# Kernel tuning notes

Measured on AMD Instinct MI355X. Metric: run time of the kernel, lower is better.

Reference implementation:

```python
import jax, jax.numpy as jnp
import numpy as np

GROUPS = 8
NUM_HEADS = 8
EPS = 1e-5


def setup_inputs() -> dict:
    key = jax.random.key(0)
    ks = jax.random.split(key, 3)
    C = 512
    x = jax.random.normal(ks[0], (2, C, 64, 64), dtype=jnp.float32)
    norm_w = jnp.ones((C,), jnp.float32)
    norm_b = jnp.zeros((C,), jnp.float32)
    qkv_w = jax.random.normal(ks[1], (3 * C, C), dtype=jnp.float32) * (C ** -0.5)
    qkv_b = jnp.zeros((3 * C,), jnp.float32)
    proj_w = jax.random.normal(ks[2], (C, C), dtype=jnp.float32) * (C ** -0.5)
    proj_b = jnp.zeros((C,), jnp.float32)
    return {"x": x, "norm_w": norm_w, "norm_b": norm_b,
            "qkv_w": qkv_w, "qkv_b": qkv_b,
            "proj_w": proj_w, "proj_b": proj_b}


def reference(x, norm_w, norm_b, qkv_w, qkv_b, proj_w, proj_b):
    b, c, h, w = x.shape
    n = h * w
    hd = c // NUM_HEADS

    # GroupNorm(8, c): normalize over (channels-in-group, h, w)
    xg = x.reshape(b, GROUPS, c // GROUPS, h, w)
    mean = jnp.mean(xg, axis=(2, 3, 4), keepdims=True)
    var = jnp.var(xg, axis=(2, 3, 4), keepdims=True)
    xg = (xg - mean) * jax.lax.rsqrt(var + EPS)
    x_norm = xg.reshape(b, c, h, w) * norm_w[None, :, None, None] + norm_b[None, :, None, None]

    x_flat = x_norm.reshape(b, c, n)  # (b, c, n)
    # 1x1 Conv1d == channel-wise linear
    qkv = jnp.einsum('oc,bcn->bon', qkv_w, x_flat) + qkv_b[None, :, None]
    q, k, v = jnp.split(qkv, 3, axis=1)
    q = q.reshape(b, NUM_HEADS, hd, n)
    k = k.reshape(b, NUM_HEADS, hd, n)
    v = v.reshape(b, NUM_HEADS, hd, n)

    attn = jnp.einsum('bhdn,bhdm->bhnm', q, k) * (hd ** -0.5)  # (b,h,n,n)
    attn = jax.nn.softmax(attn, axis=-1)
    out = jnp.einsum('bhnm,bhdm->bhdn', attn, v).reshape(b, c, n)

    out = jnp.einsum('oc,bcn->bon', proj_w, out) + proj_b[None, :, None]
    return x + out.reshape(b, c, h, w)
```

## Files before the change

### kernel.cpp

```cpp
#include <hip/hip_runtime.h>
#include <stdint.h>

#define B_   2
#define C_   512
#define N_   4096
#define G_   8
#define NH_  8
#define HD_  64
#define GRPELEMS ((C_ / G_) * N_)
#define NCHUNK 16

typedef __bf16 bf16x8 __attribute__((ext_vector_type(8)));
typedef float  f32x4  __attribute__((ext_vector_type(4)));

#if __has_builtin(__builtin_amdgcn_exp2f)
#define EXP2(x) __builtin_amdgcn_exp2f(x)
#else
#define EXP2(x) exp2f(x)
#endif

__device__ inline unsigned f2bf(float f) {
    union { float f; unsigned u; } v; v.f = f;
    return (v.u + 0x7FFFu + ((v.u >> 16) & 1u)) >> 16;
}
__device__ inline __bf16 tobf(float f) {
    unsigned short u = (unsigned short)f2bf(f);
    union { unsigned short u; __bf16 b; } c; c.u = u;
    return c.b;
}
__device__ inline unsigned pktrunc(float f0, float f1) {
    return __builtin_amdgcn_perm(__float_as_uint(f1), __float_as_uint(f0),
                                 0x07060302u);
}
__device__ inline float trunc_bf(float f) {
    return __uint_as_float(__float_as_uint(f) & 0xffff0000u);
}

#define GLOAD16(g, l)                                                     \
    __builtin_amdgcn_global_load_lds(                                     \
        (const __attribute__((address_space(1))) unsigned*)(g),           \
        (__attribute__((address_space(3))) unsigned*)(l), 16, 0, 0)

__global__ __launch_bounds__(256) void prep(const float* __restrict__ x,
                                            const float* __restrict__ qw,
                                            const float* __restrict__ pw,
                                            float* __restrict__ psum,
                                            float* __restrict__ psq,
                                            __bf16* __restrict__ dq,
                                            __bf16* __restrict__ dp) {
    const int blk = blockIdx.x;
    const int t = threadIdx.x;
    if (blk < 256) {
        const float4* p = (const float4*)x + (size_t)blk * 4096;
        float s = 0.f, s2 = 0.f;
#pragma unroll
        for (int i = 0; i < 16; ++i) {
            float4 v = p[t + (i << 8)];
            s  += v.x + v.y + v.z + v.w;
            s2 += v.x * v.x + v.y * v.y + v.z * v.z + v.w * v.w;
        }
#pragma unroll
        for (int off = 1; off < 64; off <<= 1) {
            s  += __shfl_xor(s, off);
            s2 += __shfl_xor(s2, off);
        }
        __shared__ float rs[4], rq[4];
        if ((t & 63) == 0) { rs[t >> 6] = s; rq[t >> 6] = s2; }
        __syncthreads();
        if (t == 0) {
            psum[blk] = rs[0] + rs[1] + rs[2] + rs[3];
            psq[blk]  = rq[0] + rq[1] + rq[2] + rq[3];
        }
    } else {
        const int QW4 = (3 * C_ * C_) / 4;
        int idx = (blk - 256) * 256 + t;
        float4 v; __bf16* dst; int o;
        if (idx < QW4) { v = ((const float4*)qw)[idx]; dst = dq; o = idx; }
        else           { v = ((const float4*)pw)[idx - QW4]; dst = dp; o = idx - QW4; }
        uint2 pk;
        pk.x = f2bf(v.x) | (f2bf(v.y) << 16);
        pk.y = f2bf(v.z) | (f2bf(v.w) << 16);
        *(uint2*)(dst + (size_t)o * 4) = pk;
    }
}

__global__ __launch_bounds__(256) void gn_apply_t(const float* __restrict__ x,
                                                  const float* __restrict__ w,
                                                  const float* __restrict__ bb,
                                                  const float* __restrict__ psum,
                                                  const float* __restrict__ psq,
                                                  __bf16* __restrict__ xnT) {
    const int p0 = blockIdx.x << 6, c0 = blockIdx.y << 6, b = blockIdx.z;
    __shared__ __bf16 T[64][76];
    __shared__ float red[2 * NCHUNK];
    __shared__ float smr[2];
    const int tid = threadIdx.x;
    const int bg = b * G_ + (c0 >> 6);

    if (tid < NCHUNK)            red[tid] = psum[bg * NCHUNK + tid];
    else if (tid < 2 * NCHUNK)   red[tid] = psq[bg * NCHUNK + tid - NCHUNK];
    __syncthreads();
    if (tid == 0) {
        float s = 0.f, q = 0.f;
#pragma unroll
        for (int i = 0; i < NCHUNK; ++i) { s += red[i]; q += red[NCHUNK + i]; }
        const float inv = 1.f / (float)GRPELEMS;
        float mean = s * inv;
        float var  = q * inv - mean * mean;
        smr[0] = mean;
        smr[1] = rsqrtf(var + 1e-5f);
    }
    __syncthreads();
    const float mean = smr[0], rstd = smr[1];

    const int tr  = tid >> 4;
    const int tc4 = (tid & 15) << 2;
    const float* xb = x + ((size_t)b * C_ + c0) * N_ + p0;
#pragma unroll
    for (int cc = tr; cc < 64; cc += 16) {
        int c = c0 + cc;
        float sc = rstd * w[c];
        float sh = bb[c] - mean * sc;
        float4 v = *(const float4*)(xb + (size_t)cc * N_ + tc4);
        T[tc4 + 0][cc] = tobf(v.x * sc + sh);
        T[tc4 + 1][cc] = tobf(v.y * sc + sh);
        T[tc4 + 2][cc] = tobf(v.z * sc + sh);
        T[tc4 + 3][cc] = tobf(v.w * sc + sh);
    }
    __syncthreads();
    __bf16* dst = xnT + ((size_t)b * N_ + p0) * C_ + c0;
#pragma unroll
    for (int pp = tr; pp < 64; pp += 16)
        *(uint2*)(dst + (size_t)pp * C_ + tc4) = *(const uint2*)&T[pp][tc4];
}

template <int M_TOTAL, int EPI>
__global__ __launch_bounds__(256) void gemm_bf16(const __bf16* __restrict__ A,
                                                 const __bf16* __restrict__ Bm,
                                                 const float* __restrict__ bias,
                                                 const float* __restrict__ resid,
                                                 __bf16* __restrict__ qT,
                                                 __bf16* __restrict__ kP,
                                                 __bf16* __restrict__ vP,
                                                 float* __restrict__ Y) {
    const int b  = blockIdx.z;
    const int M0 = blockIdx.y << 7;
    const int N0 = blockIdx.x << 7;
    const int tid = threadIdx.x;
    const int w = tid >> 6, lane = tid & 63;
    const int quad = lane >> 4, l16 = lane & 15;
    const int wr = w >> 1, wc = w & 1;

    __shared__ __bf16 As[128 * 64];
    __shared__ __bf16 Bs[128 * 64];

    const __bf16* Bb = Bm + (size_t)b * ((size_t)N_ * C_);

    const int srow = lane >> 3;
    const int sg   = lane & 7;

    f32x4 acc[4][4];
#pragma unroll
    for (int mt = 0; mt < 4; ++mt)
#pragma unroll
        for (int nt = 0; nt < 4; ++nt) acc[mt][nt] = (f32x4){0.f, 0.f, 0.f, 0.f};

    for (int k0 = 0; k0 < C_; k0 += 64) {
        __syncthreads();
#pragma unroll
        for (int i = 0; i < 4; ++i) {
            int r  = (w << 5) + (i << 3) + srow;
            int gc = ((sg ^ (r & 7)) << 3);
            const __bf16* ga = A  + (size_t)(M0 + r) * C_ + k0 + gc;
            const __bf16* gb = Bb + (size_t)(N0 + r) * C_ + k0 + gc;
            GLOAD16(ga, As + (((w << 2) + i) << 9));
            GLOAD16(gb, Bs + (((w << 2) + i) << 9));
        }
        __syncthreads();

#pragma unroll
        for (int kk = 0; kk < 2; ++kk) {
            bf16x8 af[4], bfr[4];
            const int gk = (kk << 2) + quad;
#pragma unroll
            for (int mt = 0; mt < 4; ++mt) {
                int m = (wr << 6) + (mt << 4) + l16;
                af[mt] = *(const bf16x8*)&As[(m << 6) + ((gk ^ (m & 7)) << 3)];
            }
#pragma unroll
            for (int nt = 0; nt < 4; ++nt) {
                int n = (wc << 6) + (nt << 4) + l16;
                bfr[nt] = *(const bf16x8*)&Bs[(n << 6) + ((gk ^ (n & 7)) << 3)];
            }
#pragma unroll
            for (int mt = 0; mt < 4; ++mt)
#pragma unroll
                for (int nt = 0; nt < 4; ++nt)
                    acc[mt][nt] = __builtin_amdgcn_mfma_f32_16x16x32_bf16(
                        af[mt], bfr[nt], acc[mt][nt], 0, 0, 0);
        }
    }

    if (EPI == 0) {
        const int t = M0 >> 9;
        const float sc = (t == 0) ? (0.125f * 1.44269504f) : 1.f;
#pragma unroll
        for (int mt = 0; mt < 4; ++mt) {
            const int o0 = M0 + (wr << 6) + (mt << 4) + (quad << 2);
            const int h  = (o0 >> 6) & 7;
            const int d0 = o0 & 63;
            const size_t bh = (size_t)b * NH_ + h;
            float bi[4];
#pragma unroll
            for (int r = 0; r < 4; ++r) bi[r] = bias[o0 + r];
            if (t == 0) {
                __bf16* dst = qT + (bh * N_) * HD_ + d0;
#pragma unroll
                for (int nt = 0; nt < 4; ++nt) {
                    int p = N0 + (wc << 6) + (nt << 4) + l16;
                    f32x4 v = acc[mt][nt];
                    uint2 pk;
                    pk.x = f2bf((v[0] + bi[0]) * sc) | (f2bf((v[1] + bi[1]) * sc) << 16);
                    pk.y = f2bf((v[2] + bi[2]) * sc) | (f2bf((v[3] + bi[3]) * sc) << 16);
                    *(uint2*)(dst + (size_t)p * HD_) = pk;
                }
            } else if (t == 1) {
                __bf16* dst = kP + bh * ((size_t)N_ * HD_);
                const size_t kkbase = (size_t)(d0 >> 3) * N_;
                const int rem = d0 & 7;
#pragma unroll
                for (int nt = 0; nt < 4; ++nt) {
                    int p = N0 + (wc << 6) + (nt << 4) + l16;
                    f32x4 v = acc[mt][nt];
                    uint2 pk;
                    pk.x = f2bf(v[0] + bi[0]) | (f2bf(v[1] + bi[1]) << 16);
                    pk.y = f2bf(v[2] + bi[2]) | (f2bf(v[3] + bi[3]) << 16);
                    *(uint2*)(dst + (kkbase + p) * 8 + rem) = pk;
                }
            } else {
                __bf16* dst = vP + bh * ((size_t)HD_ * N_);
#pragma unroll
                for (int nt = 0; nt < 4; ++nt) {
                    int p = N0 + (wc << 6) + (nt << 4) + l16;
                    const size_t gb2 = ((size_t)(p >> 3) * HD_) * 8 + (p & 7);
                    f32x4 v = acc[mt][nt];
#pragma unroll
                    for (int r = 0; r < 4; ++r)
                        dst[gb2 + (size_t)(d0 + r) * 8] = tobf(v[r] + bi[r]);
                }
            }
        }
    } else {
#pragma unroll
        for (int mt = 0; mt < 4; ++mt) {
            const int o0 = M0 + (wr << 6) + (mt << 4) + (quad << 2);
            float bi[4];
#pragma unroll
            for (int r = 0; r < 4; ++r) bi[r] = bias[o0 + r];
#pragma unroll
            for (int nt = 0; nt < 4; ++nt) {
                int p = N0 + (wc << 6) + (nt << 4) + l16;
                f32x4 v = acc[mt][nt];
#pragma unroll
                for (int r = 0; r < 4; ++r) {
                    size_t off = ((size_t)b * C_ + o0 + r) * N_ + p;
                    Y[off] = v[r] + bi[r] + resid[off];
                }
            }
        }
    }
}

__global__ __launch_bounds__(256) void attn_mfma(const __bf16* __restrict__ qT,
                                                 const __bf16* __restrict__ kP,
                                                 const __bf16* __restrict__ vP,
                                                 __bf16* __restrict__ attT) {
    const int tid  = threadIdx.x;
    const int w    = tid >> 6;
    const int lane = tid & 63;
    const int quad = lane >> 4;
    const int l16  = lane & 15;
    const int l7   = l16 & 7;
    const int h = blockIdx.y, b = blockIdx.z;
    const int qw0 = (blockIdx.x << 7) + (w << 5);

    __shared__ __bf16 Ps[4][32][64];

    const size_t bh = (size_t)b * NH_ + h;
    const __bf16* qTb = qT + bh * ((size_t)N_ * HD_);
    const __bf16* kPb = kP + bh * ((size_t)N_ * HD_);
    const __bf16* vPb = vP + bh * ((size_t)HD_ * N_);

    bf16x8 qf[2][2];
#pragma unroll
    for (int qt = 0; qt < 2; ++qt)
#pragma unroll
        for (int hh = 0; hh < 2; ++hh)
            qf[qt][hh] = *(const bf16x8*)(qTb +
                (size_t)(qw0 + (qt << 4) + l16) * HD_ + (hh << 5) + (quad << 3));

#define KADDR(hh, kt, kb) (kPb + (((size_t)((hh << 2) + quad) * N_) + (kb) + ((kt) << 4) + l16) * 8)
#define VADDR(h2, dt, kb) (vPb + (((size_t)(((kb) >> 3) + ((h2) << 2) + quad) * HD_) + ((dt) << 4) + l16) * 8)

    const f32x4 zero4 = {0.f, 0.f, 0.f, 0.f};
    f32x4 o[4][2];
#pragma unroll
    for (int dt = 0; dt < 4; ++dt) { o[dt][0] = zero4; o[dt][1] = zero4; }
    float lacc[2] = {0.f, 0.f};

    bf16x8 kf[2][4];
#pragma unroll
    for (int hh = 0; hh < 2; ++hh)
#pragma unroll
        for (int kt = 0; kt < 4; ++kt)
            kf[hh][kt] = *(const bf16x8*)KADDR(hh, kt, 0);

    for (int it = 0; it < 64; ++it) {
        const int kb = it << 6;

        bf16x8 vf[2][4];
#pragma unroll
        for (int h2 = 0; h2 < 2; ++h2)
#pragma unroll
            for (int dt = 0; dt < 4; ++dt)
                vf[h2][dt] = *(const bf16x8*)VADDR(h2, dt, kb);

        f32x4 s[4][2];
#pragma unroll
        for (int kt = 0; kt < 4; ++kt) { s[kt][0] = zero4; s[kt][1] = zero4; }
#pragma unroll
        for (int hh = 0; hh < 2; ++hh)
#pragma unroll
            for (int kt = 0; kt < 4; ++kt) {
                s[kt][0] = __builtin_amdgcn_mfma_f32_16x16x32_bf16(
                    kf[hh][kt], qf[0][hh], s[kt][0], 0, 0, 0);
                s[kt][1] = __builtin_amdgcn_mfma_f32_16x16x32_bf16(
                    kf[hh][kt], qf[1][hh], s[kt][1], 0, 0, 0);
            }

#pragma unroll
        for (int qt = 0; qt < 2; ++qt)
#pragma unroll
            for (int kt = 0; kt < 4; ++kt) {
                f32x4 sv = s[kt][qt];
                float e0 = EXP2(sv[0]), e1 = EXP2(sv[1]);
                float e2 = EXP2(sv[2]), e3 = EXP2(sv[3]);
                lacc[qt] += (trunc_bf(e0) + trunc_bf(e1)) +
                            (trunc_bf(e2) + trunc_bf(e3));
                uint2 pk;
                pk.x = pktrunc(e0, e1);
                pk.y = pktrunc(e2, e3);
                *(uint2*)&Ps[w][(qt << 4) + l16]
                            [(((kt << 2) + quad) ^ (l7 << 1)) << 2] = pk;
            }

        if (it < 63) {
#pragma unroll
            for (int hh = 0; hh < 2; ++hh)
#pragma unroll
                for (int kt = 0; kt < 4; ++kt)
                    kf[hh][kt] = *(const bf16x8*)KADDR(hh, kt, kb + 64);
        }

#pragma unroll
        for (int hh = 0; hh < 2; ++hh) {
            bf16x8 pf0 = *(const bf16x8*)&Ps[w][l16]
                          [(((hh << 3) + (quad << 1)) ^ (l7 << 1)) << 2];
            bf16x8 pf1 = *(const bf16x8*)&Ps[w][16 + l16]
                          [(((hh << 3) + (quad << 1)) ^ (l7 << 1)) << 2];
#pragma unroll
            for (int dt = 0; dt < 4; ++dt) {
                o[dt][0] = __builtin_amdgcn_mfma_f32_16x16x32_bf16(
                    vf[hh][dt], pf0, o[dt][0], 0, 0, 0);
                o[dt][1] = __builtin_amdgcn_mfma_f32_16x16x32_bf16(
                    vf[hh][dt], pf1, o[dt][1], 0, 0, 0);
            }
        }
    }

    float lq[2];
#pragma unroll
    for (int qt = 0; qt < 2; ++qt) {
        float v = lacc[qt];
        v += __shfl_xor(v, 16);
        v += __shfl_xor(v, 32);
        lq[qt] = v;
    }

#pragma unroll
    for (int qt = 0; qt < 2; ++qt) {
        float inv = 1.f / lq[qt];
        int n = qw0 + (qt << 4) + l16;
        __bf16* dst = attT + ((size_t)b * N_ + n) * C_ + h * HD_ + (quad << 2);
#pragma unroll
        for (int dt = 0; dt < 4; ++dt) {
            uint2 pk;
            pk.x = f2bf(o[dt][qt][0] * inv) | (f2bf(o[dt][qt][1] * inv) << 16);
            pk.y = f2bf(o[dt][qt][2] * inv) | (f2bf(o[dt][qt][3] * inv) << 16);
            *(uint2*)(dst + (dt << 4)) = pk;
        }
    }
#undef KADDR
#undef VADDR
}

extern "C" void kernel_launch(void* const* d_in, const int* in_sizes, int n_in,
                              void* d_out, int out_size, void* d_ws, size_t ws_size,
                              hipStream_t stream) {
    const float* x      = (const float*)d_in[0];
    const float* norm_w = (const float*)d_in[1];
    const float* norm_b = (const float*)d_in[2];
    const float* qkv_w  = (const float*)d_in[3];
    const float* qkv_b  = (const float*)d_in[4];
    const float* proj_w = (const float*)d_in[5];
    const float* proj_b = (const float*)d_in[6];
    float* out = (float*)d_out;

    const size_t BCN = (size_t)B_ * C_ * N_;
    float* psum  = (float*)d_ws;
    float* psq   = psum + 256;
    __bf16* xnT  = (__bf16*)(psq + 256);
    __bf16* qT   = xnT + BCN;
    __bf16* kP   = qT + BCN;
    __bf16* vP   = kP + BCN;
    __bf16* attT = vP + BCN;
    __bf16* wq   = attT + BCN;
    __bf16* wp   = wq + (size_t)3 * C_ * C_;

    prep<<<1280, 256, 0, stream>>>(x, qkv_w, proj_w, psum, psq, wq, wp);
    gn_apply_t<<<dim3(N_ / 64, C_ / 64, B_), 256, 0, stream>>>(
        x, norm_w, norm_b, psum, psq, xnT);
    gemm_bf16<3 * C_, 0><<<dim3(N_ / 128, 3 * C_ / 128, B_), 256, 0, stream>>>(
        wq, xnT, qkv_b, nullptr, qT, kP, vP, nullptr);
    attn_mfma<<<dim3(N_ / 128, NH_, B_), 256, 0, stream>>>(qT, kP, vP, attT);
    gemm_bf16<C_, 1><<<dim3(N_ / 128, C_ / 128, B_), 256, 0, stream>>>(
        wp, attT, proj_b, x, nullptr, nullptr, nullptr, out);
}
```

Measured before the change: 215.9 us.

## Tile K/V into contiguous 64-key blocks and halve attention query tile per wave

The QKV GEMM epilogue now writes K and V in 64-key blocks of 4096 contiguous bf16 elements, so each attention iteration reads one contiguous chunk and advances the pointer. The attention kernel drops from 32 to 16 queries per wave, doubling the grid to 1024 blocks. The softmax row sum is now an extra MFMA against a ones vector instead of scalar adds plus shuffles. The smaller query tile means each K/V load feeds half as many MFMAs, so global traffic per unit of compute roughly doubles in exchange for more blocks and fewer registers per wave.

```diff
diff --git a/kernel.cpp b/kernel.cpp
--- a/kernel.cpp
+++ b/kernel.cpp
@@ -31,9 +31,6 @@
 __device__ inline unsigned pktrunc(float f0, float f1) {
     return __builtin_amdgcn_perm(__float_as_uint(f1), __float_as_uint(f0),
                                  0x07060302u);
-}
-__device__ inline float trunc_bf(float f) {
-    return __uint_as_float(__float_as_uint(f) & 0xffff0000u);
 }
 
 #define GLOAD16(g, l)                                                     \
@@ -226,8 +223,6 @@
                 }
             } else if (t == 1) {
                 __bf16* dst = kP + bh * ((size_t)N_ * HD_);
-                const size_t kkbase = (size_t)(d0 >> 3) * N_;
-                const int rem = d0 & 7;
 #pragma unroll
                 for (int nt = 0; nt < 4; ++nt) {
                     int p = N0 + (wc << 6) + (nt << 4) + l16;
@@ -235,18 +230,21 @@
                     uint2 pk;
                     pk.x = f2bf(v[0] + bi[0]) | (f2bf(v[1] + bi[1]) << 16);
                     pk.y = f2bf(v[2] + bi[2]) | (f2bf(v[3] + bi[3]) << 16);
-                    *(uint2*)(dst + (kkbase + p) * 8 + rem) = pk;
+                    size_t off = (size_t)(p >> 6) * 4096 +
+                                 (size_t)((d0 >> 3) * 64 + (p & 63)) * 8 + (d0 & 7);
+                    *(uint2*)(dst + off) = pk;
                 }
             } else {
                 __bf16* dst = vP + bh * ((size_t)HD_ * N_);
 #pragma unroll
                 for (int nt = 0; nt < 4; ++nt) {
                     int p = N0 + (wc << 6) + (nt << 4) + l16;
-                    const size_t gb2 = ((size_t)(p >> 3) * HD_) * 8 + (p & 7);
+                    size_t base = (size_t)(p >> 6) * 4096 +
+                                  (size_t)(((p >> 3) & 7) * 64) * 8 + (p & 7);
                     f32x4 v = acc[mt][nt];
 #pragma unroll
                     for (int r = 0; r < 4; ++r)
-                        dst[gb2 + (size_t)(d0 + r) * 8] = tobf(v[r] + bi[r]);
+                        dst[base + (size_t)(d0 + r) * 8] = tobf(v[r] + bi[r]);
                 }
             }
         }
@@ -282,126 +280,107 @@
     const int l16  = lane & 15;
     const int l7   = l16 & 7;
     const int h = blockIdx.y, b = blockIdx.z;
-    const int qw0 = (blockIdx.x << 7) + (w << 5);
-
-    __shared__ __bf16 Ps[4][32][64];
+    const int qw0 = (blockIdx.x << 6) + (w << 4);
+
+    __shared__ __bf16 Ps[4][16][64];
 
     const size_t bh = (size_t)b * NH_ + h;
     const __bf16* qTb = qT + bh * ((size_t)N_ * HD_);
-    const __bf16* kPb = kP + bh * ((size_t)N_ * HD_);
-    const __bf16* vPb = vP + bh * ((size_t)HD_ * N_);
-
-    bf16x8 qf[2][2];
-#pragma unroll
-    for (int qt = 0; qt < 2; ++qt)
+    const __bf16* kblk = kP + bh * ((size_t)N_ * HD_);
+    const __bf16* vblk = vP + bh * ((size_t)HD_ * N_);
+
+    const int voff0 = (quad * 64 + l16) * 8;
+    const int voff1 = ((4 + quad) * 64 + l16) * 8;
+
+    bf16x8 qf[2];
+#pragma unroll
+    for (int hh = 0; hh < 2; ++hh)
+        qf[hh] = *(const bf16x8*)(qTb +
+            (size_t)(qw0 + l16) * HD_ + (hh << 5) + (quad << 3));
+
+    bf16x8 ones;
+#pragma unroll
+    for (int i = 0; i < 8; ++i) ones[i] = (__bf16)1.0f;
+
+    const f32x4 zero4 = {0.f, 0.f, 0.f, 0.f};
+    f32x4 o[4];
+#pragma unroll
+    for (int dt = 0; dt < 4; ++dt) o[dt] = zero4;
+    f32x4 o4 = zero4;
+
+    bf16x8 kf[2][4];
+#pragma unroll
+    for (int hh = 0; hh < 2; ++hh)
+#pragma unroll
+        for (int kt = 0; kt < 4; ++kt)
+            kf[hh][kt] = *(const bf16x8*)(kblk + (hh ? voff1 : voff0) + (kt << 7));
+
+    for (int it = 0; it < 64; ++it) {
+        bf16x8 vf[2][4];
+#pragma unroll
+        for (int h2 = 0; h2 < 2; ++h2)
+#pragma unroll
+            for (int dt = 0; dt < 4; ++dt)
+                vf[h2][dt] = *(const bf16x8*)(vblk + (h2 ? voff1 : voff0) + (dt << 7));
+
+        f32x4 s[4];
+#pragma unroll
+        for (int kt = 0; kt < 4; ++kt) s[kt] = zero4;
 #pragma unroll
         for (int hh = 0; hh < 2; ++hh)
-            qf[qt][hh] = *(const bf16x8*)(qTb +
-                (size_t)(qw0 + (qt << 4) + l16) * HD_ + (hh << 5) + (quad << 3));
-
-#define KADDR(hh, kt, kb) (kPb + (((size_t)((hh << 2) + quad) * N_) + (kb) + ((kt) << 4) + l16) * 8)
-#define VADDR(h2, dt, kb) (vPb + (((size_t)(((kb) >> 3) + ((h2) << 2) + quad) * HD_) + ((dt) << 4) + l16) * 8)
-
-    const f32x4 zero4 = {0.f, 0.f, 0.f, 0.f};
-    f32x4 o[4][2];
-#pragma unroll
-    for (int dt = 0; dt < 4; ++dt) { o[dt][0] = zero4; o[dt][1] = zero4; }
-    float lacc[2] = {0.f, 0.f};
-
-    bf16x8 kf[2][4];
-#pragma unroll
-    for (int hh = 0; hh < 2; ++hh)
-#pragma unroll
-        for (int kt = 0; kt < 4; ++kt)
-            kf[hh][kt] = *(const bf16x8*)KADDR(hh, kt, 0);
-
-    for (int it = 0; it < 64; ++it) {
-        const int kb = it << 6;
-
-        bf16x8 vf[2][4];
-#pragma unroll
-        for (int h2 = 0; h2 < 2; ++h2)
+#pragma unroll
+            for (int kt = 0; kt < 4; ++kt)
+                s[kt] = __builtin_amdgcn_mfma_f32_16x16x32_bf16(
+                    kf[hh][kt], qf[hh], s[kt], 0, 0, 0);
+
+#pragma unroll
+        for (int kt = 0; kt < 4; ++kt) {
+            f32x4 sv = s[kt];
+            float e0 = EXP2(sv[0]), e1 = EXP2(sv[1]);
+            float e2 = EXP2(sv[2]), e3 = EXP2(sv[3]);
+            uint2 pk;
+            pk.x = pktrunc(e0, e1);
+            pk.y = pktrunc(e2, e3);
+            *(uint2*)&Ps[w][l16][(((kt << 2) + quad) ^ (l7 << 1)) << 2] = pk;
+        }
+
+        if (it < 63) {
+            const __bf16* knext = kblk + 4096;
+#pragma unroll
+            for (int hh = 0; hh < 2; ++hh)
+#pragma unroll
+                for (int kt = 0; kt < 4; ++kt)
+                    kf[hh][kt] = *(const bf16x8*)(knext + (hh ? voff1 : voff0) + (kt << 7));
+        }
+
+#pragma unroll
+        for (int hh = 0; hh < 2; ++hh) {
+            bf16x8 pf = *(const bf16x8*)&Ps[w][l16]
+                          [(((hh << 3) + (quad << 1)) ^ (l7 << 1)) << 2];
 #pragma unroll
             for (int dt = 0; dt < 4; ++dt)
-                vf[h2][dt] = *(const bf16x8*)VADDR(h2, dt, kb);
-
-        f32x4 s[4][2];
-#pragma unroll
-        for (int kt = 0; kt < 4; ++kt) { s[kt][0] = zero4; s[kt][1] = zero4; }
-#pragma unroll
-        for (int hh = 0; hh < 2; ++hh)
-#pragma unroll
-            for (int kt = 0; kt < 4; ++kt) {
-                s[kt][0] = __builtin_amdgcn_mfma_f32_16x16x32_bf16(
-                    kf[hh][kt], qf[0][hh], s[kt][0], 0, 0, 0);
-                s[kt][1] = __builtin_amdgcn_mfma_f32_16x16x32_bf16(
-                    kf[hh][kt], qf[1][hh], s[kt][1], 0, 0, 0);
-            }
-
-#pragma unroll
-        for (int qt = 0; qt < 2; ++qt)
-#pragma unroll
-            for (int kt = 0; kt < 4; ++kt) {
-                f32x4 sv = s[kt][qt];
-                float e0 = EXP2(sv[0]), e1 = EXP2(sv[1]);
-                float e2 = EXP2(sv[2]), e3 = EXP2(sv[3]);
-                lacc[qt] += (trunc_bf(e0) + trunc_bf(e1)) +
-                            (trunc_bf(e2) + trunc_bf(e3));
-                uint2 pk;
-                pk.x = pktrunc(e0, e1);
-                pk.y = pktrunc(e2, e3);
-                *(uint2*)&Ps[w][(qt << 4) + l16]
-                            [(((kt << 2) + quad) ^ (l7 << 1)) << 2] = pk;
-            }
-
-        if (it < 63) {
-#pragma unroll
-            for (int hh = 0; hh < 2; ++hh)
-#pragma unroll
-                for (int kt = 0; kt < 4; ++kt)
-                    kf[hh][kt] = *(const bf16x8*)KADDR(hh, kt, kb + 64);
-        }
-
-#pragma unroll
-        for (int hh = 0; hh < 2; ++hh) {
-            bf16x8 pf0 = *(const bf16x8*)&Ps[w][l16]
-                          [(((hh << 3) + (quad << 1)) ^ (l7 << 1)) << 2];
-            bf16x8 pf1 = *(const bf16x8*)&Ps[w][16 + l16]
-                          [(((hh << 3) + (quad << 1)) ^ (l7 << 1)) << 2];
-#pragma unroll
-            for (int dt = 0; dt < 4; ++dt) {
-                o[dt][0] = __builtin_amdgcn_mfma_f32_16x16x32_bf16(
-                    vf[hh][dt], pf0, o[dt][0], 0, 0, 0);
-                o[dt][1] = __builtin_amdgcn_mfma_f32_16x16x32_bf16(
-                    vf[hh][dt], pf1, o[dt][1], 0, 0, 0);
-            }
-        }
-    }
-
-    float lq[2];
-#pragma unroll
-    for (int qt = 0; qt < 2; ++qt) {
-        float v = lacc[qt];
-        v += __shfl_xor(v, 16);
-        v += __shfl_xor(v, 32);
-        lq[qt] = v;
-    }
-
-#pragma unroll
-    for (int qt = 0; qt < 2; ++qt) {
-        float inv = 1.f / lq[qt];
-        int n = qw0 + (qt << 4) + l16;
+                o[dt] = __builtin_amdgcn_mfma_f32_16x16x32_bf16(
+                    vf[hh][dt], pf, o[dt], 0, 0, 0);
+            o4 = __builtin_amdgcn_mfma_f32_16x16x32_bf16(ones, pf, o4, 0, 0, 0);
+        }
+
+        kblk += 4096;
+        vblk += 4096;
+    }
+
+    const float inv = 1.f / o4[0];
+
+    {
+        int n = qw0 + l16;
         __bf16* dst = attT + ((size_t)b * N_ + n) * C_ + h * HD_ + (quad << 2);
 #pragma unroll
         for (int dt = 0; dt < 4; ++dt) {
             uint2 pk;
-            pk.x = f2bf(o[dt][qt][0] * inv) | (f2bf(o[dt][qt][1] * inv) << 16);
-            pk.y = f2bf(o[dt][qt][2] * inv) | (f2bf(o[dt][qt][3] * inv) << 16);
+            pk.x = f2bf(o[dt][0] * inv) | (f2bf(o[dt][1] * inv) << 16);
+            pk.y = f2bf(o[dt][2] * inv) | (f2bf(o[dt][3] * inv) << 16);
             *(uint2*)(dst + (dt << 4)) = pk;
         }
     }
-#undef KADDR
-#undef VADDR
 }
 
 extern "C" void kernel_launch(void* const* d_in, const int* in_sizes, int n_in,
@@ -432,7 +411,7 @@
         x, norm_w, norm_b, psum, psq, xnT);
     gemm_bf16<3 * C_, 0><<<dim3(N_ / 128, 3 * C_ / 128, B_), 256, 0, stream>>>(
         wq, xnT, qkv_b, nullptr, qT, kP, vP, nullptr);
-    attn_mfma<<<dim3(N_ / 128, NH_, B_), 256, 0, stream>>>(qT, kP, vP, attT);
+    attn_mfma<<<dim3(N_ / 64, NH_, B_), 256, 0, stream>>>(qT, kP, vP, attT);
     gemm_bf16<C_, 1><<<dim3(N_ / 128, C_ / 128, B_), 256, 0, stream>>>(
         wp, attT, proj_b, x, nullptr, nullptr, nullptr, out);
 }
```

New measurement: 263.6 us. +22.1%, slower.

## Tile K/V into contiguous 64-key blocks and compute softmax row sums via MFMA

Applied to the files above, without the earlier changes.

Changes the K and V packed layouts so each 64-key block is a contiguous 4096-element chunk, which turns the attention loop's address math into pointer increments and keeps each iteration's loads within one contiguous region. It also removes the per-element truncate-and-add softmax denominator accumulation and the cross-lane shuffles, replacing them with an extra MFMA against a ones vector on the P tiles already held in registers. This trades VALU work for two more MFMAs per half-iteration and requires the QKV epilogue to write the new layout.

```diff
diff --git a/kernel.cpp b/kernel.cpp
--- a/kernel.cpp
+++ b/kernel.cpp
@@ -31,9 +31,6 @@
 __device__ inline unsigned pktrunc(float f0, float f1) {
     return __builtin_amdgcn_perm(__float_as_uint(f1), __float_as_uint(f0),
                                  0x07060302u);
-}
-__device__ inline float trunc_bf(float f) {
-    return __uint_as_float(__float_as_uint(f) & 0xffff0000u);
 }
 
 #define GLOAD16(g, l)                                                     \
@@ -226,8 +223,6 @@
                 }
             } else if (t == 1) {
                 __bf16* dst = kP + bh * ((size_t)N_ * HD_);
-                const size_t kkbase = (size_t)(d0 >> 3) * N_;
-                const int rem = d0 & 7;
 #pragma unroll
                 for (int nt = 0; nt < 4; ++nt) {
                     int p = N0 + (wc << 6) + (nt << 4) + l16;
@@ -235,18 +230,21 @@
                     uint2 pk;
                     pk.x = f2bf(v[0] + bi[0]) | (f2bf(v[1] + bi[1]) << 16);
                     pk.y = f2bf(v[2] + bi[2]) | (f2bf(v[3] + bi[3]) << 16);
-                    *(uint2*)(dst + (kkbase + p) * 8 + rem) = pk;
+                    size_t off = (size_t)(p >> 6) * 4096 +
+                                 (size_t)((d0 >> 3) * 64 + (p & 63)) * 8 + (d0 & 7);
+                    *(uint2*)(dst + off) = pk;
                 }
             } else {
                 __bf16* dst = vP + bh * ((size_t)HD_ * N_);
 #pragma unroll
                 for (int nt = 0; nt < 4; ++nt) {
                     int p = N0 + (wc << 6) + (nt << 4) + l16;
-                    const size_t gb2 = ((size_t)(p >> 3) * HD_) * 8 + (p & 7);
+                    size_t base = (size_t)(p >> 6) * 4096 +
+                                  (size_t)(((p >> 3) & 7) * 64) * 8 + (p & 7);
                     f32x4 v = acc[mt][nt];
 #pragma unroll
                     for (int r = 0; r < 4; ++r)
-                        dst[gb2 + (size_t)(d0 + r) * 8] = tobf(v[r] + bi[r]);
+                        dst[base + (size_t)(d0 + r) * 8] = tobf(v[r] + bi[r]);
                 }
             }
         }
@@ -287,9 +285,12 @@
     __shared__ __bf16 Ps[4][32][64];
 
     const size_t bh = (size_t)b * NH_ + h;
-    const __bf16* qTb = qT + bh * ((size_t)N_ * HD_);
-    const __bf16* kPb = kP + bh * ((size_t)N_ * HD_);
-    const __bf16* vPb = vP + bh * ((size_t)HD_ * N_);
+    const __bf16* qTb  = qT + bh * ((size_t)N_ * HD_);
+    const __bf16* kblk = kP + bh * ((size_t)N_ * HD_);
+    const __bf16* vblk = vP + bh * ((size_t)HD_ * N_);
+
+    const int voff0 = (quad * 64 + l16) * 8;
+    const int voff1 = ((4 + quad) * 64 + l16) * 8;
 
     bf16x8 qf[2][2];
 #pragma unroll
@@ -299,31 +300,30 @@
             qf[qt][hh] = *(const bf16x8*)(qTb +
                 (size_t)(qw0 + (qt << 4) + l16) * HD_ + (hh << 5) + (quad << 3));
 
-#define KADDR(hh, kt, kb) (kPb + (((size_t)((hh << 2) + quad) * N_) + (kb) + ((kt) << 4) + l16) * 8)
-#define VADDR(h2, dt, kb) (vPb + (((size_t)(((kb) >> 3) + ((h2) << 2) + quad) * HD_) + ((dt) << 4) + l16) * 8)
+    bf16x8 ones;
+#pragma unroll
+    for (int i = 0; i < 8; ++i) ones[i] = (__bf16)1.0f;
 
     const f32x4 zero4 = {0.f, 0.f, 0.f, 0.f};
     f32x4 o[4][2];
 #pragma unroll
     for (int dt = 0; dt < 4; ++dt) { o[dt][0] = zero4; o[dt][1] = zero4; }
-    float lacc[2] = {0.f, 0.f};
+    f32x4 ol[2] = {zero4, zero4};
 
     bf16x8 kf[2][4];
 #pragma unroll
     for (int hh = 0; hh < 2; ++hh)
 #pragma unroll
         for (int kt = 0; kt < 4; ++kt)
-            kf[hh][kt] = *(const bf16x8*)KADDR(hh, kt, 0);
+            kf[hh][kt] = *(const bf16x8*)(kblk + (hh ? voff1 : voff0) + (kt << 7));
 
     for (int it = 0; it < 64; ++it) {
-        const int kb = it << 6;
-
         bf16x8 vf[2][4];
 #pragma unroll
         for (int h2 = 0; h2 < 2; ++h2)
 #pragma unroll
             for (int dt = 0; dt < 4; ++dt)
-                vf[h2][dt] = *(const bf16x8*)VADDR(h2, dt, kb);
+                vf[h2][dt] = *(const bf16x8*)(vblk + (h2 ? voff1 : voff0) + (dt << 7));
 
         f32x4 s[4][2];
 #pragma unroll
@@ -345,8 +345,6 @@
                 f32x4 sv = s[kt][qt];
                 float e0 = EXP2(sv[0]), e1 = EXP2(sv[1]);
                 float e2 = EXP2(sv[2]), e3 = EXP2(sv[3]);
-                lacc[qt] += (trunc_bf(e0) + trunc_bf(e1)) +
-                            (trunc_bf(e2) + trunc_bf(e3));
                 uint2 pk;
                 pk.x = pktrunc(e0, e1);
                 pk.y = pktrunc(e2, e3);
@@ -355,11 +353,12 @@
             }
 
         if (it < 63) {
+            const __bf16* knext = kblk + 4096;
 #pragma unroll
             for (int hh = 0; hh < 2; ++hh)
 #pragma unroll
                 for (int kt = 0; kt < 4; ++kt)
-                    kf[hh][kt] = *(const bf16x8*)KADDR(hh, kt, kb + 64);
+                    kf[hh][kt] = *(const bf16x8*)(knext + (hh ? voff1 : voff0) + (kt << 7));
         }
 
 #pragma unroll
@@ -375,21 +374,17 @@
                 o[dt][1] = __builtin_amdgcn_mfma_f32_16x16x32_bf16(
                     vf[hh][dt], pf1, o[dt][1], 0, 0, 0);
             }
-        }
-    }
-
-    float lq[2];
+            ol[0] = __builtin_amdgcn_mfma_f32_16x16x32_bf16(ones, pf0, ol[0], 0, 0, 0);
+            ol[1] = __builtin_amdgcn_mfma_f32_16x16x32_bf16(ones, pf1, ol[1], 0, 0, 0);
+        }
+
+        kblk += 4096;
+        vblk += 4096;
+    }
+
 #pragma unroll
     for (int qt = 0; qt < 2; ++qt) {
-        float v = lacc[qt];
-        v += __shfl_xor(v, 16);
-        v += __shfl_xor(v, 32);
-        lq[qt] = v;
-    }
-
-#pragma unroll
-    for (int qt = 0; qt < 2; ++qt) {
-        float inv = 1.f / lq[qt];
+        float inv = 1.f / ol[qt][0];
         int n = qw0 + (qt << 4) + l16;
         __bf16* dst = attT + ((size_t)b * N_ + n) * C_ + h * HD_ + (quad << 2);
 #pragma unroll
@@ -400,8 +395,6 @@
             *(uint2*)(dst + (dt << 4)) = pk;
         }
     }
-#undef KADDR
-#undef VADDR
 }
 
 extern "C" void kernel_launch(void* const* d_in, const int* in_sizes, int n_in,
```

Measured after the change: 248.2 us. +14.9%, slower.
